# Kernel tuning notes

Measured on AMD Instinct MI355X. Metric: run time of the kernel, lower is better.

The kernel has to match this reference:

```python
import jax, jax.numpy as jnp
import numpy as np


def bilinear_align_corners(p, H, W):
    # p: [B, C, h, w] -> [B, C, H, W], matches F.interpolate(mode='bilinear', align_corners=True)
    b, c, h, w = p.shape
    ys = jnp.linspace(0.0, h - 1.0, H)
    xs = jnp.linspace(0.0, w - 1.0, W)
    y0 = jnp.floor(ys).astype(jnp.int32)
    x0 = jnp.floor(xs).astype(jnp.int32)
    y1 = jnp.minimum(y0 + 1, h - 1)
    x1 = jnp.minimum(x0 + 1, w - 1)
    wy = (ys - y0.astype(p.dtype))[:, None]          # [H,1]
    wx = (xs - x0.astype(p.dtype))                   # [W]
    rows = p[:, :, y0, :] * (1 - wy) + p[:, :, y1, :] * wy   # [B,C,H,w]
    out = rows[:, :, :, x0] * (1 - wx) + rows[:, :, :, x1] * wx  # [B,C,H,W]
    return out


def conv1x1(x, W, b):
    return jnp.einsum('bchw,oc->bohw', x, W) + b[None, :, None, None]


def scan_axis(feat, A_bar, B_bar, axis):
    # selective recurrence h_i = A_i * stop_grad(h_{i-1}) + B_i * x_i along `axis`
    f = jnp.moveaxis(feat, axis, 0)
    A = jnp.moveaxis(A_bar, axis, 0)
    B = jnp.moveaxis(B_bar, axis, 0)

    def step(prev, inp):
        a_i, b_i, x_i = inp
        h = a_i * jax.lax.stop_gradient(prev) + b_i * x_i
        return h, h

    _, hs = jax.lax.scan(step, jnp.zeros_like(f[0]), (A, B, f))
    return jnp.moveaxis(hs, 0, axis)


def setup_inputs() -> dict:
    key = jax.random.key(0)
    ks = jax.random.split(key, 12)
    Bsz, Cin, H, W = 4, 64, 256, 256
    hid = 128
    s_in = 1.0 / np.sqrt(Cin)
    s_hid = 1.0 / np.sqrt(hid)
    return {
        'x': jax.random.normal(ks[0], (Bsz, Cin, H, W), jnp.float32),
        'prior': jax.random.normal(ks[1], (Bsz, 1, 64, 64), jnp.float32),
        'W_in': jax.random.uniform(ks[2], (hid, Cin), jnp.float32, -s_in, s_in),
        'b_in': jax.random.uniform(ks[3], (hid,), jnp.float32, -s_in, s_in),
        'W_out': jax.random.uniform(ks[4], (Cin, hid), jnp.float32, -s_hid, s_hid),
        'b_out': jax.random.uniform(ks[5], (Cin,), jnp.float32, -s_hid, s_hid),
        'W_delta': jax.random.uniform(ks[6], (hid, hid), jnp.float32, -s_hid, s_hid),
        'b_delta': jax.random.uniform(ks[7], (hid,), jnp.float32, -s_hid, s_hid),
        'W_B': jax.random.uniform(ks[8], (hid, hid), jnp.float32, -s_hid, s_hid),
        'b_B': jax.random.uniform(ks[9], (hid,), jnp.float32, -s_hid, s_hid),
        'A_param': jax.random.normal(ks[10], (hid,), jnp.float32),
        'lambda_delta': jnp.float32(0.1),
        'alpha': jnp.float32(0.1),
        'gamma': jnp.float32(0.1),
    }


def reference(x, prior, W_in, b_in, W_out, b_out, W_delta, b_delta, W_B, b_B,
              A_param, lambda_delta, alpha, gamma):
    Bsz, C, H, W = x.shape
    prior_up = jnp.clip(bilinear_align_corners(prior, H, W), -1.0, 1.0)
    x_proj = conv1x1(x, W_in, b_in)
    delta = jax.nn.softplus(conv1x1(x_proj, W_delta, b_delta) + lambda_delta * prior_up)
    B_k = conv1x1(x_proj, W_B, b_B) * (1.0 + alpha * prior_up)
    A = -jnp.exp(A_param)[None, :, None, None]
    A_bar = jnp.exp(delta * A)
    B_bar = delta * B_k
    # dim=0 in torch code scans along W (axis 3); dim=1 scans along H (axis 2)
    scanned = scan_axis(x_proj, A_bar, B_bar, 3) + scan_axis(x_proj, A_bar, B_bar, 2)
    out = conv1x1(scanned, W_out, b_out)
    return (x + gamma * out, prior_up)
```

## Files before the change

### kernel.cpp

```cpp
#include <hip/hip_runtime.h>
#include <hip/hip_bf16.h>

#define OUT1 16777216
#define BIG  33554432

typedef _Float16 half8 __attribute__((ext_vector_type(8)));
typedef float    floatx4 __attribute__((ext_vector_type(4)));

struct __align__(8) h4s { _Float16 x, y, z, w; };

__global__ __launch_bounds__(256) void k_prior(const float* __restrict__ prior, float* __restrict__ pu){
    int i = blockIdx.x*256 + threadIdx.x;
    int b = i >> 16;
    int rem = i & 65535;
    int yy = rem >> 8, xx = rem & 255;
    const float scale = 63.0f/255.0f;
    float sy = yy*scale, sx = xx*scale;
    int y0 = min((int)floorf(sy), 63), x0 = min((int)floorf(sx), 63);
    int y1 = min(y0+1, 63), x1 = min(x0+1, 63);
    float wy = sy - (float)y0, wx = sx - (float)x0;
    const float* pb = prior + (b<<12);
    float v00 = pb[(y0<<6)+x0], v01 = pb[(y0<<6)+x1];
    float v10 = pb[(y1<<6)+x0], v11 = pb[(y1<<6)+x1];
    float r0 = v00*(1.f-wy) + v10*wy;
    float r1 = v01*(1.f-wy) + v11*wy;
    float v  = r0*(1.f-wx) + r1*wx;
    pu[i] = fminf(fmaxf(v, -1.f), 1.f);
}

__global__ __launch_bounds__(256) void k_comb(const float* __restrict__ W_in, const float* __restrict__ b_in,
        const float* __restrict__ W_delta, const float* __restrict__ b_delta,
        const float* __restrict__ W_B, const float* __restrict__ b_B,
        const float* __restrict__ A_param, const float* __restrict__ W_out,
        _Float16* __restrict__ Wch, float* __restrict__ bcv, float* __restrict__ negA,
        _Float16* __restrict__ Wof, float* __restrict__ bct){
    int i = blockIdx.x*256 + threadIdx.x;
    if (i < 24576){
        int r = i >> 6, c = i & 63;
        float v;
        if (r < 128) v = W_in[i];
        else if (r < 256){
            int rr = r-128; float s = 0.f;
            for (int k=0;k<128;k++) s = fmaf(W_delta[(rr<<7)+k], W_in[(k<<6)+c], s);
            v = s;
        } else {
            int rr = r-256; float s = 0.f;
            for (int k=0;k<128;k++) s = fmaf(W_B[(rr<<7)+k], W_in[(k<<6)+c], s);
            v = s;
        }
        Wch[i] = (_Float16)v;
    } else if (i < 24960){
        int r = i - 24576; float v;
        if (r < 128) v = b_in[r];
        else if (r < 256){
            int rr=r-128; float s = b_delta[rr];
            for (int k=0;k<128;k++) s = fmaf(W_delta[(rr<<7)+k], b_in[k], s);
            v = s;
        } else {
            int rr=r-256; float s = b_B[rr];
            for (int k=0;k<128;k++) s = fmaf(W_B[(rr<<7)+k], b_in[k], s);
            v = s;
        }
        bcv[r] = v;
    } else if (i < 25088){
        negA[i-24960] = -expf(A_param[i-24960]);
    } else if (i < 33280){
        Wof[i-25088] = (_Float16)W_out[i-25088];
    } else if (i < 33792){
        int j = i - 33280;
        int c = j >> 2, comp = j & 3;
        float v;
        if (comp == 0) v = b_in[c];
        else if (comp == 1){
            float s = b_delta[c];
            for (int k=0;k<128;k++) s = fmaf(W_delta[(c<<7)+k], b_in[k], s);
            v = s;
        } else if (comp == 2){
            float s = b_B[c];
            for (int k=0;k<128;k++) s = fmaf(W_B[(c<<7)+k], b_in[k], s);
            v = s;
        } else {
            v = -expf(A_param[c]);
        }
        bct[j] = v;
    }
}

__global__ __launch_bounds__(512, 4) void k_proj_mfma(const float* __restrict__ x, const float* __restrict__ pu,
        const _Float16* __restrict__ Wch, const float* __restrict__ bct,
        const float* __restrict__ lam_p, const float* __restrict__ alp_p,
        _Float16* __restrict__ Ab, _Float16* __restrict__ Uu){
    __shared__ _Float16 Ws[24576];

    const int t    = threadIdx.x;
    const int lane = t & 63;
    const int wave = t >> 6;
    const int col  = lane & 15;
    const int quad = lane >> 4;

    const int bl      = blockIdx.x;
    const int b       = bl >> 7;
    const int px_base = (bl & 127) << 9;

    {
        const float4* wsrc = (const float4*)Wch;
        #pragma unroll
        for (int i = 0; i < 6; i++){
            int c = t + (i << 9);
            int row = c >> 3, part = c & 7;
            float4 v = wsrc[c];
            int byteoff = ((row << 7) + (part << 4)) ^ ((row & 7) << 4);
            *(float4*)((char*)Ws + byteoff) = v;
        }
    }

    const float lamv = lam_p[0], alpv = alp_p[0];
    const float* xcol = x + ((size_t)b<<22) + col;

    float xf0[8], xf1[8];
    {
        const float* xp = xcol + px_base + (wave<<4);
        #pragma unroll
        for (int j = 0; j < 8; j++){
            xf0[j] = xp[(size_t)(quad*8 + j) << 16];
            xf1[j] = xp[(size_t)(quad*8 + j + 32) << 16];
        }
    }

    __syncthreads();

    const int qb = quad << 4;
    const char* wsb = (const char*)Ws;

    #pragma unroll 1
    for (int ch = 0; ch < 4; ch++){
        const int pxw = px_base + (ch << 7) + (wave << 4);

        half8 aX0, aX1;
        #pragma unroll
        for (int j = 0; j < 8; j++){
            aX0[j] = (_Float16)xf0[j];
            aX1[j] = (_Float16)xf1[j];
        }

        if (ch < 3){
            const float* xn = xcol + pxw + 128;
            #pragma unroll
            for (int j = 0; j < 8; j++){
                xf0[j] = xn[(size_t)(quad*8 + j) << 16];
                xf1[j] = xn[(size_t)(quad*8 + j + 32) << 16];
            }
        }

        float4 puv4 = *(const float4*)(pu + (b<<16) + pxw + (quad<<2));
        float lpu[4], apu[4];
        #pragma unroll
        for (int r = 0; r < 4; r++){
            float pv = ((const float*)&puv4)[r];
            lpu[r] = lamv * pv;
            apu[r] = fmaf(alpv, pv, 1.f);
        }

        #pragma unroll 2
        for (int ct = 0; ct < 8; ct++){
            int rI = (ct << 4) + col;
            int xr = (rI & 7) << 4;
            half8 wI0 = *(const half8*)(wsb + ((( rI       << 7) +      qb) ^ xr));
            half8 wI1 = *(const half8*)(wsb + ((( rI       << 7) + 64 + qb) ^ xr));
            half8 wD0 = *(const half8*)(wsb + ((((rI + 128)<< 7) +      qb) ^ xr));
            half8 wD1 = *(const half8*)(wsb + ((((rI + 128)<< 7) + 64 + qb) ^ xr));
            half8 wB0 = *(const half8*)(wsb + ((((rI + 256)<< 7) +      qb) ^ xr));
            half8 wB1 = *(const half8*)(wsb + ((((rI + 256)<< 7) + 64 + qb) ^ xr));

            floatx4 aI = (floatx4){0.f,0.f,0.f,0.f};
            floatx4 aD = (floatx4){0.f,0.f,0.f,0.f};
            floatx4 aB = (floatx4){0.f,0.f,0.f,0.f};
            aI = __builtin_amdgcn_mfma_f32_16x16x32_f16(aX0, wI0, aI, 0, 0, 0);
            aD = __builtin_amdgcn_mfma_f32_16x16x32_f16(aX0, wD0, aD, 0, 0, 0);
            aB = __builtin_amdgcn_mfma_f32_16x16x32_f16(aX0, wB0, aB, 0, 0, 0);
            aI = __builtin_amdgcn_mfma_f32_16x16x32_f16(aX1, wI1, aI, 0, 0, 0);
            aD = __builtin_amdgcn_mfma_f32_16x16x32_f16(aX1, wD1, aD, 0, 0, 0);
            aB = __builtin_amdgcn_mfma_f32_16x16x32_f16(aX1, wB1, aB, 0, 0, 0);

            int c = (ct<<4) + col;
            float4 bv = *(const float4*)(bct + (c<<2));
            h4s oa, ou;
            #pragma unroll
            for (int r = 0; r < 4; r++){
                float sI = aI[r] + bv.x;
                float sD = aD[r] + bv.y;
                float sB = aB[r] + bv.z;
                float dpre  = sD + lpu[r];
                float delta = fmaxf(dpre, 0.f) + __logf(1.f + __expf(-fabsf(dpre)));
                float ab    = __expf(bv.w * delta);
                float uu    = delta * sB * apu[r] * sI;
                (&oa.x)[r] = (_Float16)ab;
                (&ou.x)[r] = (_Float16)uu;
            }
            size_t o = ((size_t)((b<<7) + c)<<16) + pxw + (quad<<2);
            *(h4s*)(Ab+o) = oa;
            *(h4s*)(Uu+o) = ou;
        }
    }
}

__global__ __launch_bounds__(512) void k_scan_wh(const _Float16* __restrict__ Ab, const _Float16* __restrict__ Uu,
                                                 _Float16* __restrict__ Sh){
    __shared__ float As[8][256], Us[8][256], Wsc[8][256];

    const int t    = threadIdx.x;
    const int lane = t & 63;
    const int wave = t >> 6;
    const size_t plane = (size_t)blockIdx.x << 16;

    float Hcol = 0.f;

    size_t rb = plane + ((size_t)wave << 8) + (lane << 2);
    h4s a4 = *(const h4s*)(Ab + rb);
    h4s u4 = *(const h4s*)(Uu + rb);

    #pragma unroll 1
    for (int g = 0; g < 32; g++){
        float ax=(float)a4.x, ay=(float)a4.y, az=(float)a4.z, aw=(float)a4.w;
        float ux=(float)u4.x, uy=(float)u4.y, uz=(float)u4.z, uw=(float)u4.w;

        if (g < 31){
            size_t nb = plane + (((size_t)((g+1)<<3) + wave) << 8) + (lane << 2);
            a4 = *(const h4s*)(Ab + nb);
            u4 = *(const h4s*)(Uu + nb);
        }

        float A = ax, U = ux;
        U = fmaf(ay, U, uy); A *= ay;
        U = fmaf(az, U, uz); A *= az;
        U = fmaf(aw, U, uw); A *= aw;
        #pragma unroll
        for (int off=1; off<64; off<<=1){
            float Apv = __shfl_up(A, off, 64);
            float Upv = __shfl_up(U, off, 64);
            if (lane >= off){ U = fmaf(A, Upv, U); A *= Apv; }
        }
        float h = __shfl_up(U, 1, 64);
        if (lane == 0) h = 0.f;
        float4 o;
        h = fmaf(ax, h, ux); o.x = h;
        h = fmaf(ay, h, uy); o.y = h;
        h = fmaf(az, h, uz); o.z = h;
        h = fmaf(aw, h, uw); o.w = h;

        int c0 = lane << 2;
        *(float4*)&As [wave][c0] = (float4){ax,ay,az,aw};
        *(float4*)&Us [wave][c0] = (float4){ux,uy,uz,uw};
        *(float4*)&Wsc[wave][c0] = o;
        __syncthreads();

        if (t < 256){
            size_t sb = plane + ((size_t)(g<<3) << 8) + t;
            #pragma unroll
            for (int v = 0; v < 8; v++){
                Hcol = fmaf(As[v][t], Hcol, Us[v][t]);
                Sh[sb + ((size_t)v<<8)] = (_Float16)(Hcol + Wsc[v][t]);
            }
        }
        __syncthreads();
    }
}

__global__ __launch_bounds__(256, 4) void k_out_mfma(const float* __restrict__ x, const _Float16* __restrict__ Sh,
        const _Float16* __restrict__ Wof, const float* __restrict__ bout, const float* __restrict__ gam_p,
        float* __restrict__ out){
    const int t    = threadIdx.x;
    const int lane = t & 63;
    const int wave = t >> 6;
    const int col  = lane & 15;
    const int quad = lane >> 4;
    const int b    = blockIdx.x >> 8;
    const int p0   = (blockIdx.x & 255) << 8;
    const int wn0  = wave << 6;

    const _Float16* shb = Sh + ((size_t)b<<23) + p0 + wn0;

    floatx4 acc[4][4];
    #pragma unroll
    for (int mt = 0; mt < 4; mt++)
        #pragma unroll
        for (int nt = 0; nt < 4; nt++)
            acc[mt][nt] = (floatx4){0.f,0.f,0.f,0.f};

    #pragma unroll
    for (int kc = 0; kc < 4; kc++){
        half8 af[4];
        #pragma unroll
        for (int mt = 0; mt < 4; mt++)
            #pragma unroll
            for (int j = 0; j < 8; j++)
                af[mt][j] = shb[((size_t)(kc*32 + quad*8 + j)<<16) + mt*16 + col];
        half8 bf[4];
        #pragma unroll
        for (int nt = 0; nt < 4; nt++)
            bf[nt] = *(const half8*)(Wof + (nt*16 + col)*128 + kc*32 + quad*8);
        #pragma unroll
        for (int mt = 0; mt < 4; mt++)
            #pragma unroll
            for (int nt = 0; nt < 4; nt++)
                acc[mt][nt] = __builtin_amdgcn_mfma_f32_16x16x32_f16(af[mt], bf[nt], acc[mt][nt], 0, 0, 0);
    }

    const float gv = gam_p[0];
    #pragma unroll
    for (int nt = 0; nt < 4; nt++){
        int o = nt*16 + col;
        float bo = bout[o];
        #pragma unroll
        for (int mt = 0; mt < 4; mt++){
            size_t idx = (((size_t)(b*64 + o))<<16) + p0 + wn0 + mt*16 + (quad<<2);
            float4 xv = *(const float4*)(x + idx);
            float4 ov;
            ov.x = fmaf(gv, acc[mt][nt][0] + bo, xv.x);
            ov.y = fmaf(gv, acc[mt][nt][1] + bo, xv.y);
            ov.z = fmaf(gv, acc[mt][nt][2] + bo, xv.z);
            ov.w = fmaf(gv, acc[mt][nt][3] + bo, xv.w);
            *(float4*)(out + idx) = ov;
        }
    }
}

extern "C" void kernel_launch(void* const* d_in, const int* in_sizes, int n_in,
                              void* d_out, int out_size, void* d_ws, size_t ws_size,
                              hipStream_t stream){
    const float* x       = (const float*)d_in[0];
    const float* prior   = (const float*)d_in[1];
    const float* W_in    = (const float*)d_in[2];
    const float* b_in    = (const float*)d_in[3];
    const float* W_out   = (const float*)d_in[4];
    const float* b_out   = (const float*)d_in[5];
    const float* W_delta = (const float*)d_in[6];
    const float* b_delta = (const float*)d_in[7];
    const float* W_B     = (const float*)d_in[8];
    const float* b_B     = (const float*)d_in[9];
    const float* A_param = (const float*)d_in[10];
    const float* lam     = (const float*)d_in[11];
    const float* alp     = (const float*)d_in[12];
    const float* gam     = (const float*)d_in[13];

    float* out = (float*)d_out;
    float* pu  = out + OUT1;

    float* ws        = (float*)d_ws;
    _Float16* Wch    = (_Float16*)ws;
    float* bcv       = ws + 12288;
    float* negA      = ws + 12672;
    _Float16* Wof    = (_Float16*)(ws + 12800);
    float* bct       = ws + 16896;
    _Float16* AbH    = (_Float16*)(ws + 32768);
    _Float16* UuH    = AbH + BIG;
    _Float16* Sh     = UuH + BIG;

    hipLaunchKernelGGL(k_prior,  dim3(1024),  dim3(256), 0, stream, prior, pu);
    hipLaunchKernelGGL(k_comb,   dim3(132),   dim3(256), 0, stream, W_in, b_in, W_delta, b_delta,
                       W_B, b_B, A_param, W_out, Wch, bcv, negA, Wof, bct);
    hipLaunchKernelGGL(k_proj_mfma, dim3(512), dim3(512), 0, stream,
                       x, pu, Wch, bct, lam, alp, AbH, UuH);
    hipLaunchKernelGGL(k_scan_wh, dim3(512), dim3(512), 0, stream, AbH, UuH, Sh);
    hipLaunchKernelGGL(k_out_mfma, dim3(1024), dim3(256), 0, stream, x, Sh, Wof, b_out, gam, out);
}
```

Before: 284.1 us.

## Interleave A/U intermediates, stage scan output in LDS, double-buffer loads

The projection kernel now writes A_bar and U as one interleaved 16-byte record per 4 pixels instead of two separate fp16 planes, so the scan kernel issues a single 16-byte load per lane. The scan kernel keeps two loads in flight, unrolling by two, and replaces __syncthreads with explicit lgkmcnt waits and s_barrier. Column-scan results are staged in shared memory and written back as 8-byte vectors by all waves rather than as scalar fp16 stores from half the threads. The aim is fewer and wider global memory transactions and better latency hiding, at the cost of extra LDS traffic and a hand-written barrier sequence.

```diff
diff --git a/kernel.cpp b/kernel.cpp
--- a/kernel.cpp
+++ b/kernel.cpp
@@ -8,6 +8,7 @@
 typedef float    floatx4 __attribute__((ext_vector_type(4)));
 
 struct __align__(8) h4s { _Float16 x, y, z, w; };
+struct __align__(16) au16 { h4s a, u; };
 
 __global__ __launch_bounds__(256) void k_prior(const float* __restrict__ prior, float* __restrict__ pu){
     int i = blockIdx.x*256 + threadIdx.x;
@@ -89,7 +90,7 @@
 __global__ __launch_bounds__(512, 4) void k_proj_mfma(const float* __restrict__ x, const float* __restrict__ pu,
         const _Float16* __restrict__ Wch, const float* __restrict__ bct,
         const float* __restrict__ lam_p, const float* __restrict__ alp_p,
-        _Float16* __restrict__ Ab, _Float16* __restrict__ Uu){
+        au16* __restrict__ AU){
     __shared__ _Float16 Ws[24576];
 
     const int t    = threadIdx.x;
@@ -184,7 +185,7 @@
 
             int c = (ct<<4) + col;
             float4 bv = *(const float4*)(bct + (c<<2));
-            h4s oa, ou;
+            au16 ov;
             #pragma unroll
             for (int r = 0; r < 4; r++){
                 float sI = aI[r] + bv.x;
@@ -194,41 +195,34 @@
                 float delta = fmaxf(dpre, 0.f) + __logf(1.f + __expf(-fabsf(dpre)));
                 float ab    = __expf(bv.w * delta);
                 float uu    = delta * sB * apu[r] * sI;
-                (&oa.x)[r] = (_Float16)ab;
-                (&ou.x)[r] = (_Float16)uu;
+                (&ov.a.x)[r] = (_Float16)ab;
+                (&ov.u.x)[r] = (_Float16)uu;
             }
-            size_t o = ((size_t)((b<<7) + c)<<16) + pxw + (quad<<2);
-            *(h4s*)(Ab+o) = oa;
-            *(h4s*)(Uu+o) = ou;
-        }
-    }
-}
-
-__global__ __launch_bounds__(512) void k_scan_wh(const _Float16* __restrict__ Ab, const _Float16* __restrict__ Uu,
-                                                 _Float16* __restrict__ Sh){
+            size_t u = (((size_t)((b<<7) + c)) << 14) + (pxw >> 2) + quad;
+            AU[u] = ov;
+        }
+    }
+}
+
+__global__ __launch_bounds__(512) void k_scan_wh(const au16* __restrict__ AU, _Float16* __restrict__ Sh){
     __shared__ float As[8][256], Us[8][256], Wsc[8][256];
+    __shared__ _Float16 Shs[8][256];
 
     const int t    = threadIdx.x;
     const int lane = t & 63;
     const int wave = t >> 6;
-    const size_t plane = (size_t)blockIdx.x << 16;
+    const size_t plane = (size_t)blockIdx.x;
 
     float Hcol = 0.f;
 
-    size_t rb = plane + ((size_t)wave << 8) + (lane << 2);
-    h4s a4 = *(const h4s*)(Ab + rb);
-    h4s u4 = *(const h4s*)(Uu + rb);
-
-    #pragma unroll 1
-    for (int g = 0; g < 32; g++){
-        float ax=(float)a4.x, ay=(float)a4.y, az=(float)a4.z, aw=(float)a4.w;
-        float ux=(float)u4.x, uy=(float)u4.y, uz=(float)u4.z, uw=(float)u4.w;
-
-        if (g < 31){
-            size_t nb = plane + (((size_t)((g+1)<<3) + wave) << 8) + (lane << 2);
-            a4 = *(const h4s*)(Ab + nb);
-            u4 = *(const h4s*)(Uu + nb);
-        }
+    const size_t ub = (plane << 14) + (wave << 6) + lane;
+
+    au16 cA = AU[ub];
+    au16 cB = AU[ub + 512];
+
+    auto proc = [&](au16 cur, int gg){
+        float ax=(float)cur.a.x, ay=(float)cur.a.y, az=(float)cur.a.z, aw=(float)cur.a.w;
+        float ux=(float)cur.u.x, uy=(float)cur.u.y, uz=(float)cur.u.z, uw=(float)cur.u.w;
 
         float A = ax, U = ux;
         U = fmaf(ay, U, uy); A *= ay;
@@ -252,17 +246,35 @@
         *(float4*)&As [wave][c0] = (float4){ax,ay,az,aw};
         *(float4*)&Us [wave][c0] = (float4){ux,uy,uz,uw};
         *(float4*)&Wsc[wave][c0] = o;
-        __syncthreads();
+
+        asm volatile("s_waitcnt lgkmcnt(0)" ::: "memory");
+        __builtin_amdgcn_sched_barrier(0);
+        __builtin_amdgcn_s_barrier();
+        __builtin_amdgcn_sched_barrier(0);
 
         if (t < 256){
-            size_t sb = plane + ((size_t)(g<<3) << 8) + t;
             #pragma unroll
             for (int v = 0; v < 8; v++){
                 Hcol = fmaf(As[v][t], Hcol, Us[v][t]);
-                Sh[sb + ((size_t)v<<8)] = (_Float16)(Hcol + Wsc[v][t]);
+                Shs[v][t] = (_Float16)(Hcol + Wsc[v][t]);
             }
         }
-        __syncthreads();
+
+        asm volatile("s_waitcnt lgkmcnt(0)" ::: "memory");
+        __builtin_amdgcn_sched_barrier(0);
+        __builtin_amdgcn_s_barrier();
+        __builtin_amdgcn_sched_barrier(0);
+
+        h4s sv = *(h4s*)&Shs[wave][lane << 2];
+        *(h4s*)(Sh + (plane << 16) + ((size_t)((gg << 3) + wave) << 8) + (lane << 2)) = sv;
+    };
+
+    #pragma unroll 1
+    for (int g = 0; g < 32; g += 2){
+        proc(cA, g);
+        if (g + 2 < 32) cA = AU[ub + (size_t)(g + 2) * 512];
+        proc(cB, g + 1);
+        if (g + 3 < 32) cB = AU[ub + (size_t)(g + 3) * 512];
     }
 }
 
@@ -352,15 +364,14 @@
     float* negA      = ws + 12672;
     _Float16* Wof    = (_Float16*)(ws + 12800);
     float* bct       = ws + 16896;
-    _Float16* AbH    = (_Float16*)(ws + 32768);
-    _Float16* UuH    = AbH + BIG;
-    _Float16* Sh     = UuH + BIG;
+    au16* AU         = (au16*)(ws + 32768);
+    _Float16* Sh     = (_Float16*)(AU + BIG/4);
 
     hipLaunchKernelGGL(k_prior,  dim3(1024),  dim3(256), 0, stream, prior, pu);
     hipLaunchKernelGGL(k_comb,   dim3(132),   dim3(256), 0, stream, W_in, b_in, W_delta, b_delta,
                        W_B, b_B, A_param, W_out, Wch, bcv, negA, Wof, bct);
     hipLaunchKernelGGL(k_proj_mfma, dim3(512), dim3(512), 0, stream,
-                       x, pu, Wch, bct, lam, alp, AbH, UuH);
-    hipLaunchKernelGGL(k_scan_wh, dim3(512), dim3(512), 0, stream, AbH, UuH, Sh);
+                       x, pu, Wch, bct, lam, alp, AU);
+    hipLaunchKernelGGL(k_scan_wh, dim3(512), dim3(512), 0, stream, AU, Sh);
     hipLaunchKernelGGL(k_out_mfma, dim3(1024), dim3(256), 0, stream, x, Sh, Wof, b_out, gam, out);
 }
```

New measurement: 272.5 us. -4.1%, faster.
